# Kernel optimization log

Hardware: AMD Instinct MI355X
Metric: run time of the kernel (lower is better)

The kernel has to match this reference:

```python
import math
import jax, jax.numpy as jnp
import numpy as np
from jax import lax

PI = math.pi

def _gauss1d(ks, sigma):
    # kornia gaussian: centered at (ks-1)/2 for both odd and even ks
    x = jnp.arange(ks, dtype=jnp.float32) - (ks - 1) / 2.0
    g = jnp.exp(-0.5 * (x / sigma) ** 2)
    return g / g.sum()

def _unfold_nonoverlap(x, k):
    # F.unfold(x, kernel_size=k, stride=k) for x (B,1,H,W), H,W divisible by k
    B, C, H, W = x.shape
    nH, nW = H // k, W // k
    p = x.reshape(B, nH, k, nW, k).transpose(0, 2, 4, 1, 3)
    return p.reshape(B, k * k, nH * nW)

def _sift(x, ps, nab=8, nsb=4, clipval=0.2, eps=1e-10):
    # kornia SIFTDescriptor(patch_size=ps), x: (N,1,ps,ps) -> (N,128)
    N = x.shape[0]
    g1 = _gauss1d(ps, ps / math.sqrt(2.0))
    gk = jnp.outer(g1, g1)  # (ps,ps), sum 1
    # spatial_gradient mode='diff', normalized, replicate pad
    xp = jnp.pad(x, ((0, 0), (0, 0), (0, 0), (1, 1)), mode='edge')
    gx = 0.5 * (xp[..., 2:] - xp[..., :-2])
    yp = jnp.pad(x, ((0, 0), (0, 0), (1, 1), (0, 0)), mode='edge')
    gy = 0.5 * (yp[:, :, 2:, :] - yp[:, :, :-2, :])
    mag = jnp.sqrt(gx * gx + gy * gy + eps) * gk  # (N,1,ps,ps)
    ori = jnp.arctan2(gy, gx + eps) + 2.0 * PI
    o_big = nab * ori / (2.0 * PI)
    bo0f = jnp.floor(o_big)
    w1 = o_big - bo0f
    bo0 = bo0f.astype(jnp.int32) % nab
    bo1 = (bo0 + 1) % nab
    c0 = jax.nn.one_hot(bo0[:, 0], nab, axis=1, dtype=x.dtype)  # (N,8,ps,ps)
    c1 = jax.nn.one_hot(bo1[:, 0], nab, axis=1, dtype=x.dtype)
    bins = c0 * ((1.0 - w1) * mag) + c1 * (w1 * mag)  # (N,8,ps,ps)
    # triangular pooling kernel, depthwise conv over the 8 angular bins
    bk = 2 * (ps // (nsb + 1)); stride = ps // nsb; pad = bk // 4
    half = bk / 2.0
    xc2 = half - jnp.abs(jnp.arange(bk, dtype=jnp.float32) + 0.5 - half)
    pk = jnp.outer(xc2, xc2) / (half * half)
    pk = jnp.tile(pk[None, None], (nab, 1, 1, 1))  # (8,1,bk,bk)
    pooled = lax.conv_general_dilated(bins, pk, (stride, stride),
        [(pad, pad), (pad, pad)], feature_group_count=nab,
        dimension_numbers=('NCHW', 'OIHW', 'NCHW'))  # (N,8,4,4)
    d = pooled.reshape(N, -1)
    d = d / jnp.maximum(jnp.linalg.norm(d, axis=1, keepdims=True), 1e-12)
    d = jnp.clip(d, 0.0, clipval)
    d = d / jnp.maximum(jnp.linalg.norm(d, axis=1, keepdims=True), 1e-12)
    d = jnp.sqrt(d / jnp.maximum(jnp.abs(d).sum(1, keepdims=True), 1e-12) + eps)  # rootsift
    return d

def _conv_t(x, w, b, stride=2, pad=1):
    # torch ConvTranspose2d; w: (Cin,Cout,k,k)
    k = w.shape[-1]
    wT = jnp.transpose(jnp.flip(w, (-2, -1)), (1, 0, 2, 3))  # (Cout,Cin,k,k)
    y = lax.conv_general_dilated(x, wT, (1, 1),
        [(k - 1 - pad, k - 1 - pad)] * 2, lhs_dilation=(stride, stride),
        dimension_numbers=('NCHW', 'OIHW', 'NCHW'))
    return y + b[None, :, None, None]

def _gn(x, groups, w, b, eps=1e-5):
    N, C, H, W = x.shape
    xg = x.reshape(N, groups, -1)
    mean = xg.mean(-1, keepdims=True)
    var = ((xg - mean) ** 2).mean(-1, keepdims=True)
    xn = ((xg - mean) * lax.rsqrt(var + eps)).reshape(N, C, H, W)
    return xn * w[None, :, None, None] + b[None, :, None, None]

def _jbf(x, guide, ky, kx, sigma_color, sy, sx):
    # kornia joint_bilateral_blur, border='reflect', color_distance='l1'
    B, C, H, W = x.shape
    py, px = ky // 2, kx // 2
    xp = jnp.pad(x, ((0, 0), (0, 0), (py, py), (px, px)), mode='reflect')
    gp = jnp.pad(guide, ((0, 0), (0, 0), (py, py), (px, px)), mode='reflect')
    def win(p):
        return jnp.stack([p[:, :, i:i + H, j:j + W] for i in range(ky) for j in range(kx)], axis=-1)
    ux, ug = win(xp), win(gp)  # (B,C,H,W,ky*kx)
    diff = ug - guide[..., None]
    cd2 = jnp.square(jnp.sum(jnp.abs(diff), axis=1, keepdims=True))
    ck = jnp.exp((-0.5 / (sigma_color ** 2)) * cd2)  # (B,1,H,W,K)
    sk = jnp.outer(_gauss1d(ky, sy), _gauss1d(kx, sx)).reshape(1, 1, 1, 1, -1)
    kern = sk * ck
    return (ux * kern).sum(-1) / kern.sum(-1)

def _forward(x, d1w, d1b, g1w, g1b, s1w, s1b, d2w, d2b, g2w, g2b, s2w, s2b,
             d3w, d3b, g3w, g3b, d4w, d4b, g4w, g4b, fw, fb):
    B = x.shape[0]
    s7 = _sift(_unfold_nonoverlap(x, 7).reshape(-1, 1, 32, 32), 32).reshape(B, 128, 7, 7)
    h = jax.nn.relu(_gn(_conv_t(s7, d1w, d1b), 8, g1w, g1b))  # (B,32,14,14); dropout=identity (eval)
    s14 = _sift(_unfold_nonoverlap(x, 14).reshape(-1, 1, 16, 16), 16).reshape(B, 128, 14, 14)
    sk1 = jnp.einsum('bchw,oc->bohw', s14, s1w[:, :, 0, 0]) + s1b[None, :, None, None]
    h = jax.nn.relu(_gn(_conv_t(jnp.concatenate([h, sk1], 1), d2w, d2b), 4, g2w, g2b))  # (B,16,28,28)
    s28 = _sift(_unfold_nonoverlap(x, 28).reshape(-1, 1, 8, 8), 8).reshape(B, 128, 28, 28)
    sk2 = jnp.einsum('bchw,oc->bohw', s28, s2w[:, :, 0, 0]) + s2b[None, :, None, None]
    h = jax.nn.relu(_gn(_conv_t(jnp.concatenate([h, sk2], 1), d3w, d3b), 2, g3w, g3b))  # (B,8,56,56)
    h = jax.nn.relu(_gn(_conv_t(h, d4w, d4b), 1, g4w, g4b))  # (B,4,112,112)
    h = _conv_t(h, fw, fb)  # (B,2,224,224)
    h = _jbf(h, jnp.tile(x, (1, 2, 1, 1)), 5, 5, 0.1, 1.5, 1.5)
    scale = jnp.array([0.436, 0.615], dtype=h.dtype)
    return jnp.tanh(h) * scale[None, :, None, None]

def setup_inputs() -> dict:
    key = jax.random.key(0)
    ks = jax.random.split(key, 8)
    B = 16
    f32 = jnp.float32
    def rn(k, shp, s=0.05):
        return jax.random.normal(k, shp, f32) * s
    return {
        'x': jax.random.uniform(ks[0], (B, 1, 224, 224), f32),
        'd1w': rn(ks[1], (128, 32, 4, 4)), 'd1b': jnp.zeros((32,), f32),
        'g1w': jnp.ones((32,), f32), 'g1b': jnp.zeros((32,), f32),
        's1w': rn(ks[2], (32, 128, 1, 1)), 's1b': jnp.zeros((32,), f32),
        'd2w': rn(ks[3], (64, 16, 4, 4)), 'd2b': jnp.zeros((16,), f32),
        'g2w': jnp.ones((16,), f32), 'g2b': jnp.zeros((16,), f32),
        's2w': rn(ks[4], (16, 128, 1, 1)), 's2b': jnp.zeros((16,), f32),
        'd3w': rn(ks[5], (32, 8, 4, 4)), 'd3b': jnp.zeros((8,), f32),
        'g3w': jnp.ones((8,), f32), 'g3b': jnp.zeros((8,), f32),
        'd4w': rn(ks[6], (8, 4, 4, 4)), 'd4b': jnp.zeros((4,), f32),
        'g4w': jnp.ones((4,), f32), 'g4b': jnp.zeros((4,), f32),
        'fw': rn(ks[7], (4, 2, 4, 4)), 'fb': jnp.zeros((2,), f32),
    }

def reference(x, d1w, d1b, g1w, g1b, s1w, s1b, d2w, d2b, g2w, g2b, s2w, s2b,
              d3w, d3b, g3w, g3b, d4w, d4b, g4w, g4b, fw, fb):
    return _forward(x, d1w, d1b, g1w, g1b, s1w, s1b, d2w, d2b, g2w, g2b, s2w, s2b,
                    d3w, d3b, g3w, g3b, d4w, d4b, g4w, g4b, fw, fb)
```

## Files before the change

kernel.cpp:

```cpp
#include <hip/hip_runtime.h>
#include <math.h>

#define PI_F 3.14159265358979323846f

template<int PS, int K>
__device__ __forceinline__
void sift_block(const float* __restrict__ x, float* __restrict__ out,
                int n, float* lds)
{
    constexpr int NT = 256;
    constexpr int NPIX = PS*PS;
    constexpr int BK = 2*(PS/5);
    constexpr int STRIDE = PS/4;
    constexpr int PAD = BK/4;
    constexpr float HALF = BK*0.5f;
    constexpr int NWAVE = NT/64;
    constexpr int ROWS = BK/2;

    float* patch = lds;
    float* bins  = patch + NPIX;
    float* g1    = bins + 8*NPIX;
    float* pool2 = g1 + PS;
    float* wred  = pool2 + 128;
    float* gsum_s = wred + NWAVE;

    const int tid = threadIdx.x;
    const int b = n / (K*K);
    const int c = n % (K*K);
    const int ki = c / K;
    const int kj = c % K;

    const float* xb = x + (size_t)b*224*224;
    for (int idx = tid; idx < NPIX; idx += NT) {
        int i = idx / PS, j = idx - i*PS;
        patch[idx] = xb[(i*K + ki)*224 + (j*K + kj)];
    }
    if (tid < PS) {
        const float sigma = (float)PS * 0.70710678118654752440f;
        float xv = (float)tid - (PS-1)*0.5f;
        float t = xv / sigma;
        g1[tid] = expf(-0.5f*t*t);
    }
    for (int idx = tid; idx < 8*NPIX; idx += NT) bins[idx] = 0.f;
    __syncthreads();
    if (tid == 0) {
        float s = 0.f;
        for (int i = 0; i < PS; i++) s += g1[i];
        gsum_s[0] = s;
    }
    __syncthreads();
    const float ginv = 1.0f / (gsum_s[0]*gsum_s[0]);

    for (int idx = tid; idx < NPIX; idx += NT) {
        int i = idx / PS, j = idx - i*PS;
        int jm = j > 0 ? j-1 : 0, jp = j < PS-1 ? j+1 : PS-1;
        int im = i > 0 ? i-1 : 0, ip = i < PS-1 ? i+1 : PS-1;
        float gx = 0.5f*(patch[i*PS+jp] - patch[i*PS+jm]);
        float gy = 0.5f*(patch[ip*PS+j] - patch[im*PS+j]);
        float mag = sqrtf(gx*gx + gy*gy + 1e-10f) * (g1[i]*g1[j]*ginv);
        float ori = atan2f(gy, gx + 1e-10f) + 2.f*PI_F;
        float obig = ori * (8.f/(2.f*PI_F));
        float bo0f = floorf(obig);
        float w1 = obig - bo0f;
        int bo0 = ((int)bo0f) & 7;
        int bo1 = (bo0 + 1) & 7;
        bins[bo0*NPIX + idx] = (1.f - w1)*mag;
        bins[bo1*NPIX + idx] = w1*mag;
    }
    __syncthreads();

    float pacc = 0.f;
    const int t = tid & 127;
    const int half = tid >> 7;
    {
        int o = t >> 4;
        int py = (t >> 2) & 3;
        int px = t & 3;
        int sy = py*STRIDE - PAD;
        int sx = px*STRIDE - PAD;
        const float* bo = bins + o*NPIX;
        for (int dr = 0; dr < ROWS; dr++) {
            int di = half*ROWS + dr;
            int i = sy + di;
            if (i < 0 || i >= PS) continue;
            float wi = HALF - fabsf((float)di + 0.5f - HALF);
            for (int dj = 0; dj < BK; dj++) {
                int j = sx + dj;
                if (j < 0 || j >= PS) continue;
                float wj = HALF - fabsf((float)dj + 0.5f - HALF);
                pacc += bo[i*PS + j] * (wi*wj);
            }
        }
    }
    if (half == 1) pool2[t] = pacc;
    __syncthreads();
    float d = 0.f;
    if (tid < 128) {
        d = (pacc + pool2[tid]) * (1.0f/(HALF*HALF));
    }

    const int wv = tid >> 6;
    const int ln = tid & 63;

    float v = d*d;
    #pragma unroll
    for (int off = 32; off > 0; off >>= 1) v += __shfl_down(v, off);
    if (ln == 0) wred[wv] = v;
    __syncthreads();
    float nrm = 0.f;
    #pragma unroll
    for (int w2 = 0; w2 < NWAVE; w2++) nrm += wred[w2];
    nrm = sqrtf(nrm);
    __syncthreads();
    d = d / fmaxf(nrm, 1e-12f);
    d = fminf(fmaxf(d, 0.f), 0.2f);

    v = d*d;
    #pragma unroll
    for (int off = 32; off > 0; off >>= 1) v += __shfl_down(v, off);
    if (ln == 0) wred[wv] = v;
    __syncthreads();
    nrm = 0.f;
    #pragma unroll
    for (int w2 = 0; w2 < NWAVE; w2++) nrm += wred[w2];
    nrm = sqrtf(nrm);
    __syncthreads();
    d = d / fmaxf(nrm, 1e-12f);

    v = d;
    #pragma unroll
    for (int off = 32; off > 0; off >>= 1) v += __shfl_down(v, off);
    if (ln == 0) wred[wv] = v;
    __syncthreads();
    float ssum = 0.f;
    #pragma unroll
    for (int w2 = 0; w2 < NWAVE; w2++) ssum += wred[w2];
    d = sqrtf(d / fmaxf(ssum, 1e-12f) + 1e-10f);

    if (tid < 128) out[(size_t)n*128 + tid] = d;
}

__device__ __forceinline__
void sift8_block(const float* __restrict__ x, float* __restrict__ out, int bid)
{
    const int tid = threadIdx.x;
    const int l = tid & 63;
    const int wv = tid >> 6;
    const int n = bid*4 + wv;
    const int b = n / 784;
    const int c = n % 784;
    const int ki = c / 28, kj = c % 28;
    const int i = l >> 3, j = l & 7;

    const float* xb = x + (size_t)b*50176;
    float v = xb[(i*28 + ki)*224 + (j*28 + kj)];

    int lL = (j > 0) ? l-1 : l;
    int lR = (j < 7) ? l+1 : l;
    int lU = (i > 0) ? l-8 : l;
    int lD = (i < 7) ? l+8 : l;
    float pL = __shfl(v, lL);
    float pR = __shfl(v, lR);
    float pU = __shfl(v, lU);
    float pD = __shfl(v, lD);
    float gx = 0.5f*(pR - pL);
    float gy = 0.5f*(pD - pU);

    float ti = ((float)i - 3.5f) * (1.f/5.65685424949238f);
    float tj = ((float)j - 3.5f) * (1.f/5.65685424949238f);
    float wsp = __expf(-0.5f*(ti*ti + tj*tj));
    float mag = sqrtf(gx*gx + gy*gy + 1e-10f) * wsp;
    float ori = atan2f(gy, gx + 1e-10f) + 2.f*PI_F;
    float obig = ori * (8.f/(2.f*PI_F));
    float bo0f = floorf(obig);
    float w1 = obig - bo0f;
    int bo0 = ((int)bo0f) & 7;
    int bo1 = (bo0 + 1) & 7;
    float c0 = (1.f - w1)*mag;
    float c1 = w1*mag;

    const int t = ((i & 1) << 1) | (j & 1);
    float d0 = 0.f, d1 = 0.f;
    #pragma unroll
    for (int o = 0; o < 8; o++) {
        float val = (bo0 == o ? c0 : 0.f) + (bo1 == o ? c1 : 0.f);
        val += __shfl_xor(val, 1);
        val += __shfl_xor(val, 8);
        if (o == 2*t)     d0 = val;
        if (o == 2*t + 1) d1 = val;
    }

    float s = d0*d0 + d1*d1;
    #pragma unroll
    for (int off = 32; off > 0; off >>= 1) s += __shfl_xor(s, off);
    float nrm = fmaxf(sqrtf(s), 1e-12f);
    d0 /= nrm; d1 /= nrm;
    d0 = fminf(fmaxf(d0, 0.f), 0.2f);
    d1 = fminf(fmaxf(d1, 0.f), 0.2f);
    s = d0*d0 + d1*d1;
    #pragma unroll
    for (int off = 32; off > 0; off >>= 1) s += __shfl_xor(s, off);
    nrm = fmaxf(sqrtf(s), 1e-12f);
    d0 /= nrm; d1 /= nrm;
    s = d0 + d1;
    #pragma unroll
    for (int off = 32; off > 0; off >>= 1) s += __shfl_xor(s, off);
    s = fmaxf(s, 1e-12f);
    d0 = sqrtf(d0/s + 1e-10f);
    d1 = sqrtf(d1/s + 1e-10f);

    int cell = (i >> 1)*4 + (j >> 1);
    float* ob = out + (size_t)n*128 + cell;
    ob[(2*t)*16]     = d0;
    ob[(2*t + 1)*16] = d1;
}

__global__ __launch_bounds__(256)
void sift_all(const float* __restrict__ x, float* __restrict__ s7,
              float* __restrict__ s14, float* __restrict__ s28)
{
    __shared__ float lds[9408];
    const int bid = blockIdx.x;
    if (bid < 784) {
        sift_block<32, 7>(x, s7, bid, lds);
    } else if (bid < 3920) {
        sift_block<16, 14>(x, s14, bid - 784, lds);
    } else {
        sift8_block(x, s28, bid - 3920);
    }
}

template<int CO, int S>
__device__ __forceinline__
void conv1x1_block(const float* __restrict__ in, const float* __restrict__ w,
                   const float* __restrict__ bias, float* __restrict__ out,
                   int bid, float* wt)
{
    const int tid = threadIdx.x;
    for (int i = tid; i < 128*CO; i += 256) {
        int c = i / CO, co = i - c*CO;
        wt[i] = w[co*128 + c];
    }
    __syncthreads();
    int idx = bid*256 + tid;
    int s = idx % S; int r = idx / S;
    int co4 = r % (CO/4); int b = r / (CO/4);
    int co = co4*4;
    const float* ib = in + (size_t)b*128*S + s;
    float acc0 = bias[co], acc1 = bias[co+1], acc2 = bias[co+2], acc3 = bias[co+3];
    #pragma unroll 8
    for (int c = 0; c < 128; c++) {
        float v = ib[c*S];
        const float4 wv = *(const float4*)&wt[c*CO + co];
        acc0 += v*wv.x; acc1 += v*wv.y; acc2 += v*wv.z; acc3 += v*wv.w;
    }
    float* ob = out + ((size_t)b*CO + co)*S + s;
    ob[0] = acc0; ob[S] = acc1; ob[2*S] = acc2; ob[3*S] = acc3;
}

__global__ __launch_bounds__(256)
void skip_all(const float* __restrict__ s14, const float* __restrict__ s28,
              const float* __restrict__ s1w, const float* __restrict__ s1b,
              const float* __restrict__ s2w, const float* __restrict__ s2b,
              float* __restrict__ sk1, float* __restrict__ sk2)
{
    __shared__ float wt[4096];
    const int bid = blockIdx.x;
    if (bid < 98) conv1x1_block<32, 196>(s14, s1w, s1b, sk1, bid, wt);
    else          conv1x1_block<16, 784>(s28, s2w, s2b, sk2, bid - 98, wt);
}

template<int CIN0, int CIN1, int COUT, int G, int HIN, int NCH, int RT, int NT,
         bool FUSE, int GIN, int NGIN, int NBLK_IN, int NBLK_OUT>
__global__ __launch_bounds__(NT)
void convt_tiled(const float* __restrict__ in0, const float* __restrict__ in1,
                 const float* __restrict__ w, const float* __restrict__ bias,
                 const float2* __restrict__ pst_in,
                 const float* __restrict__ gnw, const float* __restrict__ gnb,
                 float* __restrict__ out, float2* __restrict__ pst_out)
{
    constexpr int CIN = CIN0 + CIN1;
    constexpr int CG = COUT / G;
    constexpr int NGRP = NCH / CG;
    constexpr int CB = COUT / NCH;
    constexpr int H0 = 2*HIN;
    constexpr int SP = H0*H0;
    constexpr int HIN2 = HIN*HIN;
    constexpr int NR = RT/2 + 2;
    constexpr int WIN = HIN + 2;
    constexpr int TILE = CIN*NR*WIN;
    constexpr int WSTRIDE = CIN*NCH*4 + 4;
    constexpr int NPOS = RT*H0;
    constexpr int NWAVE = NT/64;

    __shared__ float tile[TILE];
    __shared__ float wl2[4*WSTRIDE];
    __shared__ float a_s[CIN0];
    __shared__ float b_s[CIN0];
    __shared__ float wpart[NWAVE][NGRP][2];

    const int tid = threadIdx.x;
    const int by = blockIdx.y;
    const int bx = blockIdx.x;
    const int b  = by / CB;
    const int cb = by - b*CB;
    const int c0 = cb*NCH;
    const int g0 = c0 / CG;
    const int r0 = bx * RT;
    const int row0 = r0/2 - 1;

    if constexpr (FUSE) {
        if (tid < CIN0) {
            int gi = tid / (CIN0/GIN);
            float s0 = 0.f, s1 = 0.f;
            for (int k = 0; k < NBLK_IN; k++) {
                float2 p = pst_in[((size_t)b*GIN + gi)*NBLK_IN + k];
                s0 += p.x; s1 += p.y;
            }
            float mean = s0 * (1.f/NGIN);
            float var  = s1 * (1.f/NGIN) - mean*mean;
            float inv  = rsqrtf(var + 1e-5f);
            float a = inv * gnw[tid];
            a_s[tid] = a;
            b_s[tid] = gnb[tid] - mean*a;
        }
        __syncthreads();
    }

    for (int idx = tid; idx < 4*CIN*NCH*4; idx += NT) {
        int k = idx & 3;
        int t2 = idx >> 2;
        int j = t2 % NCH; t2 /= NCH;
        int ci = t2 % CIN;
        int pq = t2 / CIN;
        int pA = pq >> 1, qA = pq & 1;
        int dy = pA + 2*(k>>1), dx = qA + 2*(k&1);
        wl2[pq*WSTRIDE + (ci*NCH + j)*4 + k] = w[(ci*COUT + c0 + j)*16 + dy*4 + dx];
    }

    const float* i0 = in0 + (size_t)b*CIN0*HIN2;
    for (int idx = tid; idx < TILE; idx += NT) {
        int c = idx % WIN;
        int t2 = idx / WIN;
        int r = t2 % NR;
        int ci = t2 / NR;
        int iy = row0 + r, ix = c - 1;
        float v = 0.f;
        if (iy >= 0 && iy < HIN && ix >= 0 && ix < HIN) {
            if (CIN1 == 0 || ci < CIN0) {
                v = i0[ci*HIN2 + iy*HIN + ix];
                if constexpr (FUSE) v = fmaxf(v*a_s[ci] + b_s[ci], 0.f);
            } else {
                v = in1[((size_t)b*CIN1 + (ci-CIN0))*HIN2 + iy*HIN + ix];
            }
        }
        tile[idx] = v;
    }
    __syncthreads();

    float acc[NCH];
    #pragma unroll
    for (int j = 0; j < NCH; j++) acc[j] = 0.f;

    const bool active = tid < NPOS;
    if (active) {
        int oy = r0 + tid / H0, ox = tid % H0;
        int pA = (oy+1)&1, qA = (ox+1)&1;
        int iyA = (oy+1-pA)>>1, ixA = (ox+1-qA)>>1;
        int rA = iyA - row0;
        int cA = ixA + 1;
        int toff = rA*WIN + cA;
        const float* wbase = wl2 + (pA*2+qA)*WSTRIDE;

        #pragma unroll
        for (int j = 0; j < NCH; j++) acc[j] = bias[c0 + j];

        #pragma unroll 4
        for (int ci = 0; ci < CIN; ci++) {
            const float* tp = tile + ci*(NR*WIN) + toff;
            float l0 = tp[0];
            float l1 = tp[-1];
            float l2 = tp[-WIN];
            float l3 = tp[-WIN-1];
            const float* wr = wbase + ci*NCH*4;
            #pragma unroll
            for (int j = 0; j < NCH; j++) {
                const float4 wv = *(const float4*)(wr + j*4);
                acc[j] += l0*wv.x + l1*wv.y + l2*wv.z + l3*wv.w;
            }
        }
        float* ob = out + ((size_t)b*COUT + c0)*SP + r0*H0 + tid;
        #pragma unroll
        for (int j = 0; j < NCH; j++) ob[j*SP] = acc[j];
    }

    const int wv = tid >> 6;
    const int ln = tid & 63;
    #pragma unroll
    for (int grp = 0; grp < NGRP; grp++) {
        float ps = 0.f, pq2 = 0.f;
        #pragma unroll
        for (int j = 0; j < CG; j++) {
            float v = active ? acc[grp*CG + j] : 0.f;
            ps += v; pq2 += v*v;
        }
        #pragma unroll
        for (int off = 32; off > 0; off >>= 1) {
            ps  += __shfl_down(ps,  off);
            pq2 += __shfl_down(pq2, off);
        }
        if (ln == 0) { wpart[wv][grp][0] = ps; wpart[wv][grp][1] = pq2; }
    }
    __syncthreads();
    if (tid < NGRP) {
        float s0 = 0.f, s1 = 0.f;
        #pragma unroll
        for (int w2 = 0; w2 < NWAVE; w2++) { s0 += wpart[w2][tid][0]; s1 += wpart[w2][tid][1]; }
        pst_out[((size_t)b*G + g0 + tid)*NBLK_OUT + bx] = make_float2(s0, s1);
    }
}

__global__ __launch_bounds__(256)
void final_bilateral(const float* __restrict__ h4, const float* __restrict__ fw,
                     const float* __restrict__ fb, const float2* __restrict__ pst_in,
                     const float* __restrict__ gnw, const float* __restrict__ gnb,
                     const float* __restrict__ x, float* __restrict__ out)
{
    const float g[5] = {0.1200783f, 0.2338817f, 0.2920800f, 0.2338817f, 0.1200783f};
    __shared__ float xs[400], p0s[400], p1s[400];
    __shared__ float wl2[128];
    __shared__ float a_s[4], b_s[4], bl[2], mv[2];

    const int tid = threadIdx.x;
    const int b = blockIdx.z;
    const int ty0 = blockIdx.y*16;
    const int tx0 = blockIdx.x*16;
    const float* xb = x + (size_t)b*50176;

    if (tid < 128) {
        int k = tid & 3;
        int t = tid >> 2;
        int co = t & 1; t >>= 1;
        int ci = t & 3;
        int pq = t >> 2;
        int pA = pq >> 1, qA = pq & 1;
        int dy = pA + 2*(k>>1), dx = qA + 2*(k&1);
        wl2[tid] = fw[(ci*2 + co)*16 + dy*4 + dx];
    }
    if (tid < 2) bl[tid] = fb[tid];
    if (tid >= 192) {
        int k0 = tid - 192;
        float s0 = 0.f, s1 = 0.f;
        if (k0 < 56) {
            float2 p = pst_in[(size_t)b*56 + k0];
            s0 = p.x; s1 = p.y;
        }
        #pragma unroll
        for (int off = 32; off > 0; off >>= 1) {
            s0 += __shfl_down(s0, off);
            s1 += __shfl_down(s1, off);
        }
        if (k0 == 0) {
            float mean = s0 * (1.f/50176.f);
            float var  = s1 * (1.f/50176.f) - mean*mean;
            mv[0] = mean;
            mv[1] = rsqrtf(var + 1e-5f);
        }
    }
    __syncthreads();
    if (tid < 4) {
        float a = mv[1] * gnw[tid];
        a_s[tid] = a;
        b_s[tid] = gnb[tid] - mv[0]*a;
    }
    __syncthreads();

    const float* ib = h4 + (size_t)b*4*12544;
    for (int idx = tid; idx < 400; idx += 256) {
        int r = idx / 20, cc = idx - r*20;
        int oy = ty0 - 2 + r;  oy = oy < 0 ? -oy : (oy > 223 ? 446 - oy : oy);
        int ox = tx0 - 2 + cc; ox = ox < 0 ? -ox : (ox > 223 ? 446 - ox : ox);
        xs[idx] = xb[oy*224 + ox];

        int pA = (oy+1)&1, iyA = (oy+1-pA)>>1, iyB = iyA-1;
        int qA = (ox+1)&1, ixA = (ox+1-qA)>>1, ixB = ixA-1;
        float mYA = (iyA < 112) ? 1.f : 0.f;
        float mYB = (iyB >= 0)  ? 1.f : 0.f;
        float mXA = (ixA < 112) ? 1.f : 0.f;
        float mXB = (ixB >= 0)  ? 1.f : 0.f;
        float m0 = mYA*mXA, m1 = mYA*mXB, m2 = mYB*mXA, m3 = mYB*mXB;
        int iyAc = min(iyA, 111), iyBc = max(iyB, 0);
        int ixAc = min(ixA, 111), ixBc = max(ixB, 0);
        int oAA = iyAc*112 + ixAc, oAB = iyAc*112 + ixBc;
        int oBA = iyBc*112 + ixAc, oBB = iyBc*112 + ixBc;
        const float* wbase = wl2 + (pA*2+qA)*32;

        float acc0 = bl[0], acc1 = bl[1];
        #pragma unroll
        for (int ci = 0; ci < 4; ci++) {
            const float* ip = ib + ci*12544;
            float a = a_s[ci], bb = b_s[ci];
            float l0 = fmaxf(ip[oAA]*a + bb, 0.f);
            float l1 = fmaxf(ip[oAB]*a + bb, 0.f);
            float l2 = fmaxf(ip[oBA]*a + bb, 0.f);
            float l3 = fmaxf(ip[oBB]*a + bb, 0.f);
            float t0 = l0*m0, t1 = l1*m1, t2 = l2*m2, t3 = l3*m3;
            const float4 w0 = *(const float4*)(wbase + ci*8);
            const float4 w1 = *(const float4*)(wbase + ci*8 + 4);
            acc0 += t0*w0.x + t1*w0.y + t2*w0.z + t3*w0.w;
            acc1 += t0*w1.x + t1*w1.y + t2*w1.z + t3*w1.w;
        }
        p0s[idx] = acc0;
        p1s[idx] = acc1;
    }
    __syncthreads();

    int ly = tid >> 4, lx = tid & 15;
    int base = (ly+2)*20 + (lx+2);
    float center = xs[base];
    float wsum = 0.f, a0 = 0.f, a1 = 0.f;
    #pragma unroll
    for (int di = -2; di <= 2; di++){
        #pragma unroll
        for (int dj = -2; dj <= 2; dj++){
            int o = base + di*20 + dj;
            float dg = xs[o] - center;
            float wgt = g[di+2]*g[dj+2]*__expf(-200.f*dg*dg);
            wsum += wgt;
            a0 += wgt * p0s[o];
            a1 += wgt * p1s[o];
        }
    }
    float inv = 1.0f / wsum;
    int s = (ty0 + ly)*224 + (tx0 + lx);
    out[(size_t)(b*2)*50176 + s]     = tanhf(a0*inv)*0.436f;
    out[(size_t)(b*2+1)*50176 + s]   = tanhf(a1*inv)*0.615f;
}

extern "C" void kernel_launch(void* const* d_in, const int* in_sizes, int n_in,
                              void* d_out, int out_size, void* d_ws, size_t ws_size,
                              hipStream_t stream) {
    (void)in_sizes; (void)n_in; (void)out_size; (void)ws_size;
    const float* x   = (const float*)d_in[0];
    const float* d1w = (const float*)d_in[1];
    const float* d1b = (const float*)d_in[2];
    const float* g1w = (const float*)d_in[3];
    const float* g1b = (const float*)d_in[4];
    const float* s1w = (const float*)d_in[5];
    const float* s1b = (const float*)d_in[6];
    const float* d2w = (const float*)d_in[7];
    const float* d2b = (const float*)d_in[8];
    const float* g2w = (const float*)d_in[9];
    const float* g2b = (const float*)d_in[10];
    const float* s2w = (const float*)d_in[11];
    const float* s2b = (const float*)d_in[12];
    const float* d3w = (const float*)d_in[13];
    const float* d3b = (const float*)d_in[14];
    const float* g3w = (const float*)d_in[15];
    const float* g3b = (const float*)d_in[16];
    const float* d4w = (const float*)d_in[17];
    const float* d4b = (const float*)d_in[18];
    const float* g4w = (const float*)d_in[19];
    const float* g4b = (const float*)d_in[20];
    const float* fw  = (const float*)d_in[21];
    const float* fb  = (const float*)d_in[22];
    float* out = (float*)d_out;

    float* ws  = (float*)d_ws;
    float* s7  = ws;
    float* s14 = s7  + 100352;
    float* s28 = s14 + 401408;
    float* sk1 = s28 + 1605632;
    float* sk2 = sk1 + 100352;
    float* h1  = sk2 + 200704;
    float* h2  = h1  + 100352;
    float* h3  = h2  + 200704;
    float* h4  = h3  + 401408;
    float2* pst1 = (float2*)(h4 + 802816);
    float2* pst2 = pst1 + 128;
    float2* pst3 = pst2 + 448;
    float2* pst4 = pst3 + 448;

    sift_all<<<7056, 256, 0, stream>>>(x, s7, s14, s28);

    skip_all<<<294, 256, 0, stream>>>(s14, s28, s1w, s1b, s2w, s2b, sk1, sk2);

    convt_tiled<128, 0, 32, 8,  7, 4, 14, 256, false, 1, 1, 1, 1>
        <<<dim3(1, 16*8), 256, 0, stream>>>(s7, nullptr, d1w, d1b, nullptr, nullptr, nullptr, h1, pst1);
    convt_tiled< 32,32, 16, 4, 14, 8,  4, 128, true, 8, 784, 1, 7>
        <<<dim3(7, 16*2), 128, 0, stream>>>(h1, sk1, d2w, d2b, pst1, g1w, g1b, h2, pst2);
    convt_tiled< 16,16,  8, 2, 28, 8,  4, 256, true, 4, 3136, 7, 14>
        <<<dim3(14, 16), 256, 0, stream>>>(h2, sk2, d3w, d3b, pst2, g2w, g2b, h3, pst3);
    convt_tiled<  8, 0,  4, 1, 56, 4,  2, 256, true, 2, 12544, 14, 56>
        <<<dim3(56, 16), 256, 0, stream>>>(h3, nullptr, d4w, d4b, pst3, g3w, g3b, h4, pst4);

    final_bilateral<<<dim3(14, 14, 16), 256, 0, stream>>>(h4, fw, fb, pst4, g4w, g4b, x, out);
}
```

Measured before the change: 239.8 us.

## Merge first transposed conv into skip kernel and pad SIFT bin planes

The first transposed-conv layer (128->32, 7->14) now runs inside the same launch as the two 1x1 skip convolutions, using extra blocks with a dedicated per-parity weight layout and an input tile in shared memory. This removes one kernel launch and lets the small layer run alongside the skip work. Separately, the SIFT per-bin planes are padded by one float to spread LDS bank accesses. The fused kernel now needs a larger static LDS allocation (about 74 KB), which may reduce occupancy for the skip-conv blocks.

```diff
diff --git a/kernel.cpp b/kernel.cpp
--- a/kernel.cpp
+++ b/kernel.cpp
@@ -10,6 +10,7 @@
 {
     constexpr int NT = 256;
     constexpr int NPIX = PS*PS;
+    constexpr int NPIXP = NPIX + 1;
     constexpr int BK = 2*(PS/5);
     constexpr int STRIDE = PS/4;
     constexpr int PAD = BK/4;
@@ -19,7 +20,7 @@
 
     float* patch = lds;
     float* bins  = patch + NPIX;
-    float* g1    = bins + 8*NPIX;
+    float* g1    = bins + 8*NPIXP;
     float* pool2 = g1 + PS;
     float* wred  = pool2 + 128;
     float* gsum_s = wred + NWAVE;
@@ -41,7 +42,7 @@
         float t = xv / sigma;
         g1[tid] = expf(-0.5f*t*t);
     }
-    for (int idx = tid; idx < 8*NPIX; idx += NT) bins[idx] = 0.f;
+    for (int idx = tid; idx < 8*NPIXP; idx += NT) bins[idx] = 0.f;
     __syncthreads();
     if (tid == 0) {
         float s = 0.f;
@@ -64,8 +65,8 @@
         float w1 = obig - bo0f;
         int bo0 = ((int)bo0f) & 7;
         int bo1 = (bo0 + 1) & 7;
-        bins[bo0*NPIX + idx] = (1.f - w1)*mag;
-        bins[bo1*NPIX + idx] = w1*mag;
+        bins[bo0*NPIXP + idx] = (1.f - w1)*mag;
+        bins[bo1*NPIXP + idx] = w1*mag;
     }
     __syncthreads();
 
@@ -78,7 +79,7 @@
         int px = t & 3;
         int sy = py*STRIDE - PAD;
         int sx = px*STRIDE - PAD;
-        const float* bo = bins + o*NPIX;
+        const float* bo = bins + o*NPIXP;
         for (int dr = 0; dr < ROWS; dr++) {
             int di = half*ROWS + dr;
             int i = sy + di;
@@ -258,16 +259,120 @@
     ob[0] = acc0; ob[S] = acc1; ob[2*S] = acc2; ob[3*S] = acc3;
 }
 
+__device__ __forceinline__
+void convt_l1_block(const float* __restrict__ in0, const float* __restrict__ w,
+                    const float* __restrict__ bias,
+                    float* __restrict__ out, float2* __restrict__ pst_out,
+                    int by, float* lds)
+{
+    constexpr int CIN = 128, COUT = 32, HIN = 7, NCH = 4, NT = 256;
+    constexpr int H0 = 14, SP = 196, HIN2 = 49;
+    constexpr int NR = 9, WIN = 9, TILE = CIN*NR*WIN;
+    constexpr int WSTRIDE = CIN*NCH*4 + 4;
+
+    float* tile  = lds;
+    float* wl2   = tile + TILE;
+    float* wpart = wl2 + 4*WSTRIDE;
+
+    const int tid = threadIdx.x;
+    const int b  = by >> 3;
+    const int cb = by & 7;
+    const int c0 = cb*NCH;
+
+    for (int idx = tid; idx < 4*CIN*NCH*4; idx += NT) {
+        int k = idx & 3;
+        int t2 = idx >> 2;
+        int j = t2 % NCH; t2 /= NCH;
+        int ci = t2 % CIN;
+        int pq = t2 / CIN;
+        int pA = pq >> 1, qA = pq & 1;
+        int dy = pA + 2*(k>>1), dx = qA + 2*(k&1);
+        wl2[pq*WSTRIDE + (ci*NCH + j)*4 + k] = w[(ci*COUT + c0 + j)*16 + dy*4 + dx];
+    }
+    const float* i0 = in0 + (size_t)b*CIN*HIN2;
+    for (int idx = tid; idx < TILE; idx += NT) {
+        int c = idx % WIN;
+        int t2 = idx / WIN;
+        int r = t2 % NR;
+        int ci = t2 / NR;
+        int iy = r - 1, ix = c - 1;
+        float v = 0.f;
+        if (iy >= 0 && iy < HIN && ix >= 0 && ix < HIN)
+            v = i0[ci*HIN2 + iy*HIN + ix];
+        tile[idx] = v;
+    }
+    __syncthreads();
+
+    float acc[NCH];
+    #pragma unroll
+    for (int j = 0; j < NCH; j++) acc[j] = 0.f;
+
+    const bool active = tid < SP;
+    if (active) {
+        int oy = tid / H0, ox = tid % H0;
+        int pA = (oy+1)&1, qA = (ox+1)&1;
+        int iyA = (oy+1-pA)>>1, ixA = (ox+1-qA)>>1;
+        int toff = (iyA+1)*WIN + (ixA+1);
+        const float* wbase = wl2 + (pA*2+qA)*WSTRIDE;
+
+        #pragma unroll
+        for (int j = 0; j < NCH; j++) acc[j] = bias[c0 + j];
+
+        #pragma unroll 4
+        for (int ci = 0; ci < CIN; ci++) {
+            const float* tp = tile + ci*(NR*WIN) + toff;
+            float l0 = tp[0];
+            float l1 = tp[-1];
+            float l2 = tp[-WIN];
+            float l3 = tp[-WIN-1];
+            const float* wr = wbase + ci*NCH*4;
+            #pragma unroll
+            for (int j = 0; j < NCH; j++) {
+                const float4 wv = *(const float4*)(wr + j*4);
+                acc[j] += l0*wv.x + l1*wv.y + l2*wv.z + l3*wv.w;
+            }
+        }
+        float* ob = out + ((size_t)b*COUT + c0)*SP + tid;
+        #pragma unroll
+        for (int j = 0; j < NCH; j++) ob[j*SP] = acc[j];
+    }
+
+    const int wv = tid >> 6;
+    const int ln = tid & 63;
+    float ps = 0.f, pq2 = 0.f;
+    #pragma unroll
+    for (int j = 0; j < NCH; j++) {
+        float v = active ? acc[j] : 0.f;
+        ps += v; pq2 += v*v;
+    }
+    #pragma unroll
+    for (int off = 32; off > 0; off >>= 1) {
+        ps  += __shfl_down(ps,  off);
+        pq2 += __shfl_down(pq2, off);
+    }
+    if (ln == 0) { wpart[wv*2] = ps; wpart[wv*2+1] = pq2; }
+    __syncthreads();
+    if (tid == 0) {
+        float s0 = wpart[0]+wpart[2]+wpart[4]+wpart[6];
+        float s1 = wpart[1]+wpart[3]+wpart[5]+wpart[7];
+        pst_out[(size_t)b*8 + cb] = make_float2(s0, s1);
+    }
+}
+
 __global__ __launch_bounds__(256)
-void skip_all(const float* __restrict__ s14, const float* __restrict__ s28,
-              const float* __restrict__ s1w, const float* __restrict__ s1b,
-              const float* __restrict__ s2w, const float* __restrict__ s2b,
-              float* __restrict__ sk1, float* __restrict__ sk2)
+void skip_l1(const float* __restrict__ s14, const float* __restrict__ s28,
+             const float* __restrict__ s1w, const float* __restrict__ s1b,
+             const float* __restrict__ s2w, const float* __restrict__ s2b,
+             const float* __restrict__ s7,  const float* __restrict__ d1w,
+             const float* __restrict__ d1b,
+             float* __restrict__ sk1, float* __restrict__ sk2,
+             float* __restrict__ h1, float2* __restrict__ pst1)
 {
-    __shared__ float wt[4096];
+    __shared__ float lds[18584];
     const int bid = blockIdx.x;
-    if (bid < 98) conv1x1_block<32, 196>(s14, s1w, s1b, sk1, bid, wt);
-    else          conv1x1_block<16, 784>(s28, s2w, s2b, sk2, bid - 98, wt);
+    if (bid < 98)       conv1x1_block<32, 196>(s14, s1w, s1b, sk1, bid, lds);
+    else if (bid < 294) conv1x1_block<16, 784>(s28, s2w, s2b, sk2, bid - 98, lds);
+    else                convt_l1_block(s7, d1w, d1b, h1, pst1, bid - 294, lds);
 }
 
 template<int CIN0, int CIN1, int COUT, int G, int HIN, int NCH, int RT, int NT,
@@ -583,10 +688,9 @@
 
     sift_all<<<7056, 256, 0, stream>>>(x, s7, s14, s28);
 
-    skip_all<<<294, 256, 0, stream>>>(s14, s28, s1w, s1b, s2w, s2b, sk1, sk2);
-
-    convt_tiled<128, 0, 32, 8,  7, 4, 14, 256, false, 1, 1, 1, 1>
-        <<<dim3(1, 16*8), 256, 0, stream>>>(s7, nullptr, d1w, d1b, nullptr, nullptr, nullptr, h1, pst1);
+    skip_l1<<<422, 256, 0, stream>>>(s14, s28, s1w, s1b, s2w, s2b,
+                                     s7, d1w, d1b, sk1, sk2, h1, pst1);
+
     convt_tiled< 32,32, 16, 4, 14, 8,  4, 128, true, 8, 784, 1, 7>
         <<<dim3(7, 16*2), 128, 0, stream>>>(h1, sk1, d2w, d2b, pst1, g1w, g1b, h2, pst2);
     convt_tiled< 16,16,  8, 2, 28, 8,  4, 256, true, 4, 3136, 7, 14>
```

Measured after the change: 234.1 us. 1.02x faster.
